# Kernel optimization log

Hardware: AMD Instinct MI355X
Metric: run time of the kernel (lower is better)

The kernel has to match this reference:

```python
import jax, jax.numpy as jnp
import numpy as np

N, E = 50000, 500000
SD, VD, HID, DEPTH = 128, 3, 64, 4
CUTOFF = 5.0


def setup_inputs() -> dict:
    key = jax.random.key(0)
    ks = jax.random.split(key, 13)
    s = jax.random.normal(ks[0], (N, SD), jnp.float32)
    v = jax.random.normal(ks[1], (N, VD, 3), jnp.float32)
    edge_index = jax.random.randint(ks[2], (2, E), 0, N, jnp.int32)
    d = jax.random.uniform(ks[3], (E, 1), jnp.float32) * CUTOFF  # distances within cutoff
    r = jax.random.normal(ks[4], (E, 3), jnp.float32)            # relative position vectors

    def lin(k, shp):
        return jax.random.normal(k, shp, jnp.float32) * (1.0 / np.sqrt(shp[-2]))

    # per-layer stacked parameters [DEPTH, ...]
    W1 = lin(ks[5], (DEPTH, 2 * SD + 1, HID)); b1 = jnp.zeros((DEPTH, HID), jnp.float32)
    W2 = lin(ks[6], (DEPTH, HID, HID));        b2 = jnp.zeros((DEPTH, HID), jnp.float32)
    W3 = lin(ks[7], (DEPTH, HID, SD + 2 * VD)); b3 = jnp.zeros((DEPTH, SD + 2 * VD), jnp.float32)
    Wn1 = lin(ks[8], (DEPTH, 2 * SD, HID)); bn1 = jnp.zeros((DEPTH, HID), jnp.float32)
    Wn2 = lin(ks[9], (DEPTH, HID, SD));     bn2 = jnp.zeros((DEPTH, SD), jnp.float32)
    return dict(s=s, v=v, edge_index=edge_index, d=d, r=r,
                W1=W1, b1=b1, W2=W2, b2=b2, W3=W3, b3=b3,
                Wn1=Wn1, bn1=bn1, Wn2=Wn2, bn2=bn2)


def _egnn(s, v, edge_index, d, r, W1, b1, W2, b2, W3, b3, Wn1, bn1, Wn2, bn2):
    dst, src = edge_index[0], edge_index[1]
    # cosine cutoff envelope, zero beyond CUTOFF
    C = 0.5 * (jnp.cos(jnp.pi * d / CUTOFF) + 1.0) * (d < CUTOFF)  # [E,1]
    # in-degree counts for 'mean' vector aggregation (fixed, layer-independent)
    cnt = jax.ops.segment_sum(jnp.ones((E,), jnp.float32), dst, num_segments=N)
    inv_cnt = 1.0 / jnp.maximum(cnt, 1.0)  # [N]
    for l in range(DEPTH):
        # gather + edge MLP (EGCL message)
        h = jnp.concatenate([s[dst], s[src], d], axis=-1)      # [E, 2*SD+1]
        h = jax.nn.silu(h @ W1[l] + b1[l])
        h = jax.nn.silu(h @ W2[l] + b2[l])
        m = h @ W3[l] + b3[l]                                   # [E, SD+2*VD]
        ms, gv, gr = m[:, :SD], m[:, SD:SD + VD], m[:, SD + VD:]
        ms = ms * C                                             # scalar message
        # equivariant vector message: gated source vectors + gated edge direction
        vm = (v[src] * gv[:, :, None] + r[:, None, :] * gr[:, :, None]) * C[:, :, None]
        # scatter aggregate: sum for scalars, mean for vectors (vector_aggr='mean')
        s_agg = jax.ops.segment_sum(ms, dst, num_segments=N)    # [N, SD]
        v_agg = jax.ops.segment_sum(vm, dst, num_segments=N) * inv_cnt[:, None, None]
        # node update (residual)
        u = jax.nn.silu(jnp.concatenate([s, s_agg], axis=-1) @ Wn1[l] + bn1[l])
        s = s + u @ Wn2[l] + bn2[l]
        v = v + v_agg
    return s, v


def reference(s, v, edge_index, d, r, W1, b1, W2, b2, W3, b3, Wn1, bn1, Wn2, bn2):
    return _egnn(s, v, edge_index, d, r, W1, b1, W2, b2, W3, b3, Wn1, bn1, Wn2, bn2)
```

## Files before the change

### kernel.cpp

```cpp
#include <hip/hip_runtime.h>
#include <hip/hip_bf16.h>
#include <math.h>

#define N_NODES 50000
#define N_EDGES 500000
#define SD 128
#define VD 3
#define HID 64
#define DEPTH 4

#define NF1 32
#define NF2 8
#define NF3 18
#define W1F_SH (NF1 * 512)
#define W2F_SH (NF2 * 512)
#define W3F_SH (NF3 * 512)
#define WPK_SH (W1F_SH + W2F_SH + W3F_SH)

#define WN1T_SH (64 * 256)
#define WN2T_SH (128 * 64)
#define WN_SH (WN1T_SH + WN2T_SH)

#define EDGE_GRID 512
#define NTILES (N_EDGES / 16)
#define EDGE_ITERS ((NTILES + EDGE_GRID * 4 - 1) / (EDGE_GRID * 4))

typedef __attribute__((ext_vector_type(8))) short short8;
typedef __attribute__((ext_vector_type(4))) float f32x4;

__device__ __forceinline__ float silu_f(float x) {
    return x / (1.0f + __expf(-x));
}

__device__ __forceinline__ unsigned short f2bf(float x) {
    __hip_bfloat16 h = __float2bfloat16(x);
    return *reinterpret_cast<unsigned short*>(&h);
}

__device__ __forceinline__ float bf2f(unsigned short u) {
    union { unsigned int i; float f; } c; c.i = ((unsigned int)u) << 16;
    return c.f;
}


__global__ void cast_s_kernel(const float* __restrict__ in, float* __restrict__ out,
                              unsigned short* __restrict__ out_bf, int n) {
    int i = blockIdx.x * blockDim.x + threadIdx.x;
    if (i < n) { float x = in[i]; out[i] = x; out_bf[i] = f2bf(x); }
}

__global__ void copy_kernel(const float* __restrict__ in, float* __restrict__ out, int n) {
    int i = blockIdx.x * blockDim.x + threadIdx.x;
    if (i < n) out[i] = in[i];
}

__global__ void prep_edges(const int* __restrict__ ei, const float* __restrict__ d,
                           float* __restrict__ C, int* __restrict__ cnti) {
    int e = blockIdx.x * blockDim.x + threadIdx.x;
    if (e >= N_EDGES) return;
    float de = d[e];
    float c = 0.5f * (cosf(3.14159265358979323846f * de * (1.0f / 5.0f)) + 1.0f);
    C[e] = (de < 5.0f) ? c : 0.0f;
    atomicAdd(&cnti[ei[e]], 1);
}

__global__ void inv_cnt_kernel(const int* __restrict__ cnti, float* __restrict__ inv_cnt) {
    int i = blockIdx.x * blockDim.x + threadIdx.x;
    if (i < N_NODES) inv_cnt[i] = 1.0f / fmaxf((float)cnti[i], 1.0f);
}

__global__ __launch_bounds__(1024) void scan_block(const int* __restrict__ cnti,
                                                   int* __restrict__ offs,
                                                   int* __restrict__ bsum) {
    __shared__ int sh[1024];
    int tid = threadIdx.x;
    int idx = blockIdx.x * 1024 + tid;
    int x = (idx < N_NODES) ? cnti[idx] : 0;
    sh[tid] = x;
    __syncthreads();
    for (int off = 1; off < 1024; off <<= 1) {
        int y = (tid >= off) ? sh[tid - off] : 0;
        __syncthreads();
        sh[tid] += y;
        __syncthreads();
    }
    if (idx < N_NODES) offs[idx] = sh[tid] - x;
    if (tid == 1023) bsum[blockIdx.x] = sh[1023];
}

__global__ void scan_partials(int* __restrict__ bsum, int nb, int* __restrict__ offs_total) {
    if (threadIdx.x == 0 && blockIdx.x == 0) {
        int acc = 0;
        for (int i = 0; i < nb; i++) { int t = bsum[i]; bsum[i] = acc; acc += t; }
        offs_total[0] = acc;
    }
}

__global__ __launch_bounds__(1024) void scan_apply(int* __restrict__ offs,
                                                   const int* __restrict__ bsum) {
    int idx = blockIdx.x * 1024 + threadIdx.x;
    if (idx < N_NODES) offs[idx] += bsum[blockIdx.x];
}

__global__ void build_perm(const int* __restrict__ ei, const int* __restrict__ offs,
                           int* __restrict__ cursor, int* __restrict__ eids) {
    int e = blockIdx.x * blockDim.x + threadIdx.x;
    if (e >= N_EDGES) return;
    int dst = ei[e];
    int p = offs[dst] + atomicAdd(&cursor[dst], 1);
    eids[p] = e;
}

__global__ void permute_edges(const int* __restrict__ ei, const float* __restrict__ d,
                              const float* __restrict__ C, const float* __restrict__ r,
                              const int* __restrict__ eids,
                              int* __restrict__ dst_s, int* __restrict__ src_s,
                              float* __restrict__ d_s, float* __restrict__ C_s,
                              float* __restrict__ r_s) {
    int p = blockIdx.x * blockDim.x + threadIdx.x;
    if (p >= N_EDGES) return;
    int e = eids[p];
    dst_s[p] = ei[e];
    src_s[p] = ei[N_EDGES + e];
    d_s[p] = d[e];
    C_s[p] = C[e];
    r_s[3 * (size_t)p + 0] = r[3 * (size_t)e + 0];
    r_s[3 * (size_t)p + 1] = r[3 * (size_t)e + 1];
    r_s[3 * (size_t)p + 2] = r[3 * (size_t)e + 2];
}

__global__ void prep_weights(const float* __restrict__ W1, const float* __restrict__ W2,
                             const float* __restrict__ W3, unsigned short* __restrict__ Wpk) {
    int idx = blockIdx.x * blockDim.x + threadIdx.x;
    if (idx >= DEPTH * WPK_SH) return;
    int l = idx / WPK_SH;
    int j = idx - l * WPK_SH;
    float val = 0.0f;
    if (j < W1F_SH) {
        int f = j >> 9, rrr = j & 511;
        int lane = rrr >> 3, jj = rrr & 7;
        int q = lane >> 4, lo = lane & 15;
        int ks = f >> 2, t = f & 3;
        int k = ks * 32 + q * 8 + jj;
        int n = t * 16 + lo;
        val = W1[((size_t)l * 257 + k) * 64 + n];
    } else if (j < W1F_SH + W2F_SH) {
        int jj2 = j - W1F_SH;
        int f = jj2 >> 9, rrr = jj2 & 511;
        int lane = rrr >> 3, jj = rrr & 7;
        int q = lane >> 4, lo = lane & 15;
        int ks = f >> 2, t = f & 3;
        int k = ks * 32 + q * 8 + jj;
        int n = t * 16 + lo;
        val = W2[((size_t)l * 64 + k) * 64 + n];
    } else {
        int jj3 = j - W1F_SH - W2F_SH;
        int f = jj3 >> 9, rrr = jj3 & 511;
        int lane = rrr >> 3, jj = rrr & 7;
        int q = lane >> 4, lo = lane & 15;
        int ks = f / 9, t = f - ks * 9;
        int k = ks * 32 + q * 8 + jj;
        int n = t * 16 + lo;
        val = (n < 134) ? W3[((size_t)l * 64 + k) * 134 + n] : 0.0f;
    }
    Wpk[idx] = f2bf(val);
}

__global__ void prep_node_weights(const float* __restrict__ Wn1, const float* __restrict__ Wn2,
                                  unsigned short* __restrict__ Wnpk) {
    int idx = blockIdx.x * blockDim.x + threadIdx.x;
    if (idx >= DEPTH * WN_SH) return;
    int l = idx / WN_SH;
    int j = idx - l * WN_SH;
    float val;
    if (j < WN1T_SH) {
        int n = j / 256, k = j - n * 256;
        val = Wn1[((size_t)l * 256 + k) * 64 + n];
    } else {
        int jj = j - WN1T_SH;
        int n = jj / 64, k = jj - n * 64;
        val = Wn2[((size_t)l * 64 + k) * 128 + n];
    }
    Wnpk[idx] = f2bf(val);
}

__global__ __launch_bounds__(256, 2) void edge_mfma(
    const unsigned short* __restrict__ s_bf, const float* __restrict__ v,
    const int* __restrict__ dst_s, const int* __restrict__ src_s,
    const float* __restrict__ d_s, const float* __restrict__ C_s,
    const float* __restrict__ r_s,
    const unsigned short* __restrict__ Wpk_l,
    const float* __restrict__ W1r,
    const float* __restrict__ b1, const float* __restrict__ b2,
    const float* __restrict__ b3,
    unsigned short* __restrict__ smsg, unsigned short* __restrict__ vmsg)
{
    __shared__ __align__(16) unsigned short w1f[W1F_SH];
    __shared__ __align__(16) unsigned short w3f[W3F_SH];
    __shared__ __align__(16) unsigned short Hb[4][16 * 72];
    __shared__ float gb[4][16][6];

    const int tid  = threadIdx.x;
    const int wl   = tid >> 6;
    const int lane = tid & 63;
    const int lo   = lane & 15;
    const int q    = lane >> 4;

    {
        const short8* g1 = reinterpret_cast<const short8*>(Wpk_l);
        const short8* g3 = reinterpret_cast<const short8*>(Wpk_l + W1F_SH + W2F_SH);
        short8* l1 = reinterpret_cast<short8*>(w1f);
        short8* l3 = reinterpret_cast<short8*>(w3f);
        for (int i = tid; i < W1F_SH / 8; i += 256) l1[i] = g1[i];
        for (int i = tid; i < W3F_SH / 8; i += 256) l3[i] = g3[i];
    }
    __syncthreads();

    const unsigned short* w2g = Wpk_l + W1F_SH;

    float bb1[4], wr1[4], bb2[4], bb3[9];
    #pragma unroll
    for (int t = 0; t < 4; t++) { bb1[t] = b1[t * 16 + lo]; wr1[t] = W1r[t * 16 + lo]; }
    #pragma unroll
    for (int t = 0; t < 4; t++) bb2[t] = b2[t * 16 + lo];
    #pragma unroll
    for (int t = 0; t < 9; t++) { int n = t * 16 + lo; bb3[t] = (n < 134) ? b3[n] : 0.0f; }

    int tile = blockIdx.x * 4 + wl;
    if (tile > NTILES - 1) tile = NTILES - 1;
    long eb = (long)tile * 16;
    int sn_t = 0;
    short8 ad[4], asf[4];
    float4 dd4, ce4;
    float vsr[9], rv[3], cel_t = 0.0f;
    {
        int dn = dst_s[eb + lo];
        int sn = src_s[eb + lo];
        dd4 = *reinterpret_cast<const float4*>(d_s + eb + 4 * q);
        ce4 = *reinterpret_cast<const float4*>(C_s + eb + 4 * q);
        const unsigned short* rd = s_bf + (size_t)dn * SD;
        const unsigned short* rs = s_bf + (size_t)sn * SD;
        #pragma unroll
        for (int ks = 0; ks < 4; ks++) {
            ad[ks]  = *reinterpret_cast<const short8*>(rd + ks * 32 + q * 8);
            asf[ks] = *reinterpret_cast<const short8*>(rs + ks * 32 + q * 8);
        }
        if (lane < 16) {
            sn_t = sn;
            cel_t = C_s[eb + lane];
            #pragma unroll
            for (int t = 0; t < 9; t++) vsr[t] = v[(size_t)sn * 9 + t];
            #pragma unroll
            for (int t = 0; t < 3; t++) rv[t] = r_s[3 * eb + 3 * lane + t];
        }
    }

    for (int it = 0; it < EDGE_ITERS; it++) {
        int tile_n = (it + 1) * (EDGE_GRID * 4) + blockIdx.x * 4 + wl;
        if (tile_n > NTILES - 1) tile_n = NTILES - 1;
        long ebn = (long)tile_n * 16;
        int dn_n = dst_s[ebn + lo];
        int sn_n = src_s[ebn + lo];
        float4 dd4_n = *reinterpret_cast<const float4*>(d_s + ebn + 4 * q);
        float4 ce4_n = *reinterpret_cast<const float4*>(C_s + ebn + 4 * q);
        float cel_n = 0.0f, rv_n[3];
        if (lane < 16) {
            cel_n = C_s[ebn + lane];
            #pragma unroll
            for (int t = 0; t < 3; t++) rv_n[t] = r_s[3 * ebn + 3 * lane + t];
        }

        f32x4 acc1[4];
        #pragma unroll
        for (int t = 0; t < 4; t++) {
            float dd[4] = { dd4.x, dd4.y, dd4.z, dd4.w };
            #pragma unroll
            for (int rr = 0; rr < 4; rr++) acc1[t][rr] = bb1[t] + dd[rr] * wr1[t];
        }
        #pragma unroll
        for (int ks = 0; ks < 4; ks++) {
            #pragma unroll
            for (int t = 0; t < 4; t++) {
                short8 b = *reinterpret_cast<const short8*>(&w1f[((ks * 4 + t) * 64 + lane) * 8]);
                acc1[t] = __builtin_amdgcn_mfma_f32_16x16x32_bf16(ad[ks], b, acc1[t], 0, 0, 0);
            }
        }
        #pragma unroll
        for (int ks = 0; ks < 4; ks++) {
            #pragma unroll
            for (int t = 0; t < 4; t++) {
                short8 b = *reinterpret_cast<const short8*>(&w1f[(((ks + 4) * 4 + t) * 64 + lane) * 8]);
                acc1[t] = __builtin_amdgcn_mfma_f32_16x16x32_bf16(asf[ks], b, acc1[t], 0, 0, 0);
            }
        }
        #pragma unroll
        for (int t = 0; t < 4; t++)
            #pragma unroll
            for (int rr = 0; rr < 4; rr++)
                Hb[wl][(4 * q + rr) * 72 + t * 16 + lo] = f2bf(silu_f(acc1[t][rr]));
        __syncthreads();

        short8 a2[2];
        #pragma unroll
        for (int ks = 0; ks < 2; ks++)
            a2[ks] = *reinterpret_cast<const short8*>(&Hb[wl][lo * 72 + ks * 32 + q * 8]);
        f32x4 acc2[4];
        #pragma unroll
        for (int t = 0; t < 4; t++) {
            #pragma unroll
            for (int rr = 0; rr < 4; rr++) acc2[t][rr] = bb2[t];
        }
        #pragma unroll
        for (int ks = 0; ks < 2; ks++) {
            #pragma unroll
            for (int t = 0; t < 4; t++) {
                short8 b = *reinterpret_cast<const short8*>(w2g + ((ks * 4 + t) * 64 + lane) * 8);
                acc2[t] = __builtin_amdgcn_mfma_f32_16x16x32_bf16(a2[ks], b, acc2[t], 0, 0, 0);
            }
        }

        short8 ad_n[4], as_n[4];
        {
            const unsigned short* rd = s_bf + (size_t)dn_n * SD;
            const unsigned short* rs = s_bf + (size_t)sn_n * SD;
            #pragma unroll
            for (int ks = 0; ks < 4; ks++) {
                ad_n[ks] = *reinterpret_cast<const short8*>(rd + ks * 32 + q * 8);
                as_n[ks] = *reinterpret_cast<const short8*>(rs + ks * 32 + q * 8);
            }
        }
        float vsr_n[9];
        if (lane < 16) {
            #pragma unroll
            for (int t = 0; t < 9; t++) vsr_n[t] = v[(size_t)sn_n * 9 + t];
        }

        __syncthreads();
        #pragma unroll
        for (int t = 0; t < 4; t++)
            #pragma unroll
            for (int rr = 0; rr < 4; rr++)
                Hb[wl][(4 * q + rr) * 72 + t * 16 + lo] = f2bf(silu_f(acc2[t][rr]));
        __syncthreads();

        short8 a3[2];
        #pragma unroll
        for (int ks = 0; ks < 2; ks++)
            a3[ks] = *reinterpret_cast<const short8*>(&Hb[wl][lo * 72 + ks * 32 + q * 8]);
        f32x4 acc3[9];
        #pragma unroll
        for (int t = 0; t < 9; t++) {
            #pragma unroll
            for (int rr = 0; rr < 4; rr++) acc3[t][rr] = bb3[t];
        }
        #pragma unroll
        for (int ks = 0; ks < 2; ks++) {
            #pragma unroll
            for (int t = 0; t < 9; t++) {
                short8 b = *reinterpret_cast<const short8*>(&w3f[((ks * 9 + t) * 64 + lane) * 8]);
                acc3[t] = __builtin_amdgcn_mfma_f32_16x16x32_bf16(a3[ks], b, acc3[t], 0, 0, 0);
            }
        }

        float ce[4] = { ce4.x, ce4.y, ce4.z, ce4.w };
        #pragma unroll
        for (int t = 0; t < 8; t++) {
            int colc = t * 16 + lo;
            #pragma unroll
            for (int rr = 0; rr < 4; rr++) {
                long erow = eb + 4 * q + rr;
                smsg[erow * SD + colc] = f2bf(acc3[t][rr] * ce[rr]);
            }
        }
        if (lo < 6) {
            #pragma unroll
            for (int rr = 0; rr < 4; rr++) gb[wl][4 * q + rr][lo] = acc3[8][rr];
        }
        __syncthreads();

        if (lane < 16) {
            long e = eb + lane;
            #pragma unroll
            for (int vi = 0; vi < VD; vi++) {
                float gv = gb[wl][lane][vi], gr = gb[wl][lane][VD + vi];
                vmsg[e * 12 + vi * 3 + 0] = f2bf((vsr[vi * 3 + 0] * gv + rv[0] * gr) * cel_t);
                vmsg[e * 12 + vi * 3 + 1] = f2bf((vsr[vi * 3 + 1] * gv + rv[1] * gr) * cel_t);
                vmsg[e * 12 + vi * 3 + 2] = f2bf((vsr[vi * 3 + 2] * gv + rv[2] * gr) * cel_t);
            }
        }

        eb = ebn;
        dd4 = dd4_n; ce4 = ce4_n;
        cel_t = cel_n; sn_t = sn_n;
        #pragma unroll
        for (int ks = 0; ks < 4; ks++) { ad[ks] = ad_n[ks]; asf[ks] = as_n[ks]; }
        #pragma unroll
        for (int t = 0; t < 9; t++) vsr[t] = vsr_n[t];
        #pragma unroll
        for (int t = 0; t < 3; t++) rv[t] = rv_n[t];
    }
}

__global__ __launch_bounds__(256) void agg_kernel(
    const unsigned short* __restrict__ smsg, const unsigned short* __restrict__ vmsg,
    const int* __restrict__ offs,
    unsigned short* __restrict__ s_agg_bf, float* __restrict__ v_agg)
{
    int wave = blockIdx.x * 4 + (threadIdx.x >> 6);
    int lane = threadIdx.x & 63;
    if (wave >= N_NODES) return;
    int beg = offs[wave], end = offs[wave + 1];
    float a0 = 0.0f, a1 = 0.0f, va = 0.0f;
    const ushort2* sm2 = reinterpret_cast<const ushort2*>(smsg);
    for (int i = beg; i < end; i++) {
        ushort2 mm = sm2[(size_t)i * 64 + lane];
        a0 += bf2f(mm.x);
        a1 += bf2f(mm.y);
        if (lane < 9) va += bf2f(vmsg[(size_t)i * 12 + lane]);
    }
    ushort2 o; o.x = f2bf(a0); o.y = f2bf(a1);
    *reinterpret_cast<ushort2*>(s_agg_bf + (size_t)wave * SD + lane * 2) = o;
    if (lane < 9) v_agg[(size_t)wave * 9 + lane] = va;
}

__global__ __launch_bounds__(256) void node_mfma(
    float* __restrict__ s, float* __restrict__ v, unsigned short* __restrict__ s_bf,
    const unsigned short* __restrict__ s_agg_bf, const float* __restrict__ v_agg,
    const float* __restrict__ inv_cnt,
    const unsigned short* __restrict__ Wn_l,
    const float* __restrict__ bn1, const float* __restrict__ bn2)
{
    __shared__ __align__(16) unsigned short Hb[4][16 * 72];

    const int tid  = threadIdx.x;
    const int wl   = tid >> 6;
    const int lane = tid & 63;
    const int lo   = lane & 15;
    const int q    = lane >> 4;
    const int nb   = blockIdx.x * 64 + wl * 16;

    int na = nb + lo; if (na > N_NODES - 1) na = N_NODES - 1;
    const unsigned short* rs = s_bf     + (size_t)na * SD;
    const unsigned short* ra = s_agg_bf + (size_t)na * SD;

    f32x4 acc1[4];
    #pragma unroll
    for (int t = 0; t < 4; t++) {
        float bb = bn1[t * 16 + lo];
        #pragma unroll
        for (int rr = 0; rr < 4; rr++) acc1[t][rr] = bb;
    }
    #pragma unroll
    for (int ks = 0; ks < 4; ks++) {
        short8 a = *reinterpret_cast<const short8*>(rs + ks * 32 + q * 8);
        #pragma unroll
        for (int t = 0; t < 4; t++) {
            short8 b = *reinterpret_cast<const short8*>(Wn_l + (t * 16 + lo) * 256 + ks * 32 + q * 8);
            acc1[t] = __builtin_amdgcn_mfma_f32_16x16x32_bf16(a, b, acc1[t], 0, 0, 0);
        }
    }
    #pragma unroll
    for (int ks = 0; ks < 4; ks++) {
        short8 a = *reinterpret_cast<const short8*>(ra + ks * 32 + q * 8);
        #pragma unroll
        for (int t = 0; t < 4; t++) {
            short8 b = *reinterpret_cast<const short8*>(Wn_l + (t * 16 + lo) * 256 + 128 + ks * 32 + q * 8);
            acc1[t] = __builtin_amdgcn_mfma_f32_16x16x32_bf16(a, b, acc1[t], 0, 0, 0);
        }
    }
    #pragma unroll
    for (int t = 0; t < 4; t++)
        #pragma unroll
        for (int rr = 0; rr < 4; rr++)
            Hb[wl][(4 * q + rr) * 72 + t * 16 + lo] = f2bf(silu_f(acc1[t][rr]));
    __syncthreads();

    const unsigned short* w2g = Wn_l + WN1T_SH;
    f32x4 acc2[8];
    #pragma unroll
    for (int t = 0; t < 8; t++) {
        float bb = bn2[t * 16 + lo];
        #pragma unroll
        for (int rr = 0; rr < 4; rr++) acc2[t][rr] = bb;
    }
    #pragma unroll
    for (int ks = 0; ks < 2; ks++) {
        short8 a = *reinterpret_cast<const short8*>(&Hb[wl][lo * 72 + ks * 32 + q * 8]);
        #pragma unroll
        for (int t = 0; t < 8; t++) {
            short8 b = *reinterpret_cast<const short8*>(w2g + (t * 16 + lo) * 64 + ks * 32 + q * 8);
            acc2[t] = __builtin_amdgcn_mfma_f32_16x16x32_bf16(a, b, acc2[t], 0, 0, 0);
        }
    }

    #pragma unroll
    for (int t = 0; t < 8; t++) {
        int col = t * 16 + lo;
        #pragma unroll
        for (int rr = 0; rr < 4; rr++) {
            int node = nb + 4 * q + rr;
            if (node < N_NODES) {
                size_t idx = (size_t)node * SD + col;
                float ns = s[idx] + acc2[t][rr];
                s[idx] = ns;
                s_bf[idx] = f2bf(ns);
            }
        }
    }

    if (lane < 16) {
        int node = nb + lane;
        if (node < N_NODES) {
            float ic = inv_cnt[node];
            #pragma unroll
            for (int t = 0; t < VD * 3; t++)
                v[(size_t)node * 9 + t] += v_agg[(size_t)node * 9 + t] * ic;
        }
    }
}

extern "C" void kernel_launch(void* const* d_in, const int* in_sizes, int n_in,
                              void* d_out, int out_size, void* d_ws, size_t ws_size,
                              hipStream_t stream)
{
    (void)in_sizes; (void)n_in; (void)out_size; (void)ws_size;
    const float* s_in = (const float*)d_in[0];
    const float* v_in = (const float*)d_in[1];
    const int*   ei   = (const int*)d_in[2];
    const float* d_e  = (const float*)d_in[3];
    const float* r_e  = (const float*)d_in[4];
    const float* W1   = (const float*)d_in[5];
    const float* b1   = (const float*)d_in[6];
    const float* W2   = (const float*)d_in[7];
    const float* b2   = (const float*)d_in[8];
    const float* W3   = (const float*)d_in[9];
    const float* b3   = (const float*)d_in[10];
    const float* Wn1  = (const float*)d_in[11];
    const float* bn1  = (const float*)d_in[12];
    const float* Wn2  = (const float*)d_in[13];
    const float* bn2  = (const float*)d_in[14];

    float* s = (float*)d_out;
    float* v = s + (size_t)N_NODES * SD;

    float* ws      = (float*)d_ws;
    float* v_agg   = ws;
    float* cntinv  = v_agg + (size_t)N_NODES * 9;
    float* Cbuf    = cntinv + N_NODES;
    int*   cnti    = (int*)(Cbuf + N_EDGES);
    int*   offs    = cnti + N_NODES;
    int*   cursor  = offs + N_NODES + 1;
    int*   eids    = cursor + N_NODES;
    int*   bsum    = eids + N_EDGES;
    int*   dst_s   = bsum + 64;
    int*   src_s   = dst_s + N_EDGES;
    float* d_s     = (float*)(src_s + N_EDGES);
    float* C_s     = d_s + N_EDGES;
    float* r_s     = C_s + N_EDGES;
    uintptr_t up   = (uintptr_t)(r_s + (size_t)3 * N_EDGES);
    up = (up + 15) & ~(uintptr_t)15;
    unsigned short* s_bf     = (unsigned short*)up;
    unsigned short* s_agg_bf = s_bf + (size_t)N_NODES * SD;
    unsigned short* Wpk      = s_agg_bf + (size_t)N_NODES * SD;
    unsigned short* Wnpk     = Wpk + (size_t)DEPTH * WPK_SH;
    unsigned short* smsg     = Wnpk + (size_t)DEPTH * WN_SH;
    unsigned short* vmsg     = smsg + (size_t)N_EDGES * SD;

    hipMemsetAsync(cnti, 0, sizeof(int) * (size_t)N_NODES, stream);
    hipMemsetAsync(cursor, 0, sizeof(int) * (size_t)N_NODES, stream);

    cast_s_kernel<<<(N_NODES * SD + 255) / 256, 256, 0, stream>>>(s_in, s, s_bf, N_NODES * SD);
    copy_kernel<<<(N_NODES * VD * 3 + 255) / 256, 256, 0, stream>>>(v_in, v, N_NODES * VD * 3);
    prep_edges<<<(N_EDGES + 255) / 256, 256, 0, stream>>>(ei, d_e, Cbuf, cnti);
    inv_cnt_kernel<<<(N_NODES + 255) / 256, 256, 0, stream>>>(cnti, cntinv);

    const int NB = (N_NODES + 1023) / 1024;
    scan_block<<<NB, 1024, 0, stream>>>(cnti, offs, bsum);
    scan_partials<<<1, 64, 0, stream>>>(bsum, NB, offs + N_NODES);
    scan_apply<<<NB, 1024, 0, stream>>>(offs, bsum);
    build_perm<<<(N_EDGES + 255) / 256, 256, 0, stream>>>(ei, offs, cursor, eids);
    permute_edges<<<(N_EDGES + 255) / 256, 256, 0, stream>>>(
        ei, d_e, Cbuf, r_e, eids, dst_s, src_s, d_s, C_s, r_s);

    prep_weights<<<(DEPTH * WPK_SH + 255) / 256, 256, 0, stream>>>(W1, W2, W3, Wpk);
    prep_node_weights<<<(DEPTH * WN_SH + 255) / 256, 256, 0, stream>>>(Wn1, Wn2, Wnpk);

    for (int l = 0; l < DEPTH; l++) {
        edge_mfma<<<EDGE_GRID, 256, 0, stream>>>(
            s_bf, v, dst_s, src_s, d_s, C_s, r_s,
            Wpk + (size_t)l * WPK_SH,
            W1 + ((size_t)l * 257 + 256) * 64,
            b1 + (size_t)l * HID, b2 + (size_t)l * HID, b3 + (size_t)l * (SD + 2 * VD),
            smsg, vmsg);
        agg_kernel<<<(N_NODES + 3) / 4, 256, 0, stream>>>(
            smsg, vmsg, offs, s_agg_bf, v_agg);
        node_mfma<<<(N_NODES + 63) / 64, 256, 0, stream>>>(
            s, v, s_bf, s_agg_bf, v_agg, cntinv,
            Wnpk + (size_t)l * WN_SH,
            bn1 + (size_t)l * HID, bn2 + (size_t)l * SD);
    }
}
```

Baseline: 954.9 us.

## Fuse message aggregation into edge kernel with segmented atomic adds

The edge kernel now reduces each 16-edge tile's scalar and vector messages by runs of equal destination node (edges are sorted by dst) and adds them straight into fp32 s_agg/v_agg with atomics. This removes the separate aggregation kernel and the bf16 per-edge message buffers written to and read back from global memory. The aggregate buffer is zeroed each layer with a memset, and the node kernel converts the fp32 aggregate to bf16 on load. In exchange it adds extra block barriers, atomic traffic and a serial segment loop per tile, and the order of the floating-point summation is no longer fixed.

```diff
diff --git a/kernel.cpp b/kernel.cpp
--- a/kernel.cpp
+++ b/kernel.cpp
@@ -40,6 +40,13 @@
 __device__ __forceinline__ float bf2f(unsigned short u) {
     union { unsigned int i; float f; } c; c.i = ((unsigned int)u) << 16;
     return c.f;
+}
+
+__device__ __forceinline__ short8 cvt8(const float* __restrict__ p) {
+    short8 o;
+    #pragma unroll
+    for (int i = 0; i < 8; i++) o[i] = (short)f2bf(p[i]);
+    return o;
 }
 
 
@@ -193,12 +200,14 @@
     const float* __restrict__ W1r,
     const float* __restrict__ b1, const float* __restrict__ b2,
     const float* __restrict__ b3,
-    unsigned short* __restrict__ smsg, unsigned short* __restrict__ vmsg)
+    float* __restrict__ s_agg, float* __restrict__ v_agg)
 {
     __shared__ __align__(16) unsigned short w1f[W1F_SH];
     __shared__ __align__(16) unsigned short w3f[W3F_SH];
     __shared__ __align__(16) unsigned short Hb[4][16 * 72];
     __shared__ float gb[4][16][6];
+    __shared__ float vtile[4][16][9];
+    __shared__ int tdst[4][16];
 
     const int tid  = threadIdx.x;
     const int wl   = tid >> 6;
@@ -226,19 +235,19 @@
     #pragma unroll
     for (int t = 0; t < 9; t++) { int n = t * 16 + lo; bb3[t] = (n < 134) ? b3[n] : 0.0f; }
 
-    int tile = blockIdx.x * 4 + wl;
-    if (tile > NTILES - 1) tile = NTILES - 1;
-    long eb = (long)tile * 16;
-    int sn_t = 0;
+    int raw0 = blockIdx.x * 4 + wl;
+    bool val_c = true;
+    long eb = (long)raw0 * 16;
+    int dn_c;
     short8 ad[4], asf[4];
     float4 dd4, ce4;
     float vsr[9], rv[3], cel_t = 0.0f;
     {
-        int dn = dst_s[eb + lo];
+        dn_c = dst_s[eb + lo];
         int sn = src_s[eb + lo];
         dd4 = *reinterpret_cast<const float4*>(d_s + eb + 4 * q);
         ce4 = *reinterpret_cast<const float4*>(C_s + eb + 4 * q);
-        const unsigned short* rd = s_bf + (size_t)dn * SD;
+        const unsigned short* rd = s_bf + (size_t)dn_c * SD;
         const unsigned short* rs = s_bf + (size_t)sn * SD;
         #pragma unroll
         for (int ks = 0; ks < 4; ks++) {
@@ -246,7 +255,6 @@
             asf[ks] = *reinterpret_cast<const short8*>(rs + ks * 32 + q * 8);
         }
         if (lane < 16) {
-            sn_t = sn;
             cel_t = C_s[eb + lane];
             #pragma unroll
             for (int t = 0; t < 9; t++) vsr[t] = v[(size_t)sn * 9 + t];
@@ -256,8 +264,9 @@
     }
 
     for (int it = 0; it < EDGE_ITERS; it++) {
-        int tile_n = (it + 1) * (EDGE_GRID * 4) + blockIdx.x * 4 + wl;
-        if (tile_n > NTILES - 1) tile_n = NTILES - 1;
+        int raw_n = (it + 1) * (EDGE_GRID * 4) + blockIdx.x * 4 + wl;
+        bool val_n = (raw_n < NTILES);
+        int tile_n = val_n ? raw_n : (NTILES - 1);
         long ebn = (long)tile_n * 16;
         int dn_n = dst_s[ebn + lo];
         int sn_n = src_s[ebn + lo];
@@ -362,36 +371,58 @@
             }
         }
 
-        float ce[4] = { ce4.x, ce4.y, ce4.z, ce4.w };
-        #pragma unroll
-        for (int t = 0; t < 8; t++) {
-            int colc = t * 16 + lo;
-            #pragma unroll
-            for (int rr = 0; rr < 4; rr++) {
-                long erow = eb + 4 * q + rr;
-                smsg[erow * SD + colc] = f2bf(acc3[t][rr] * ce[rr]);
-            }
-        }
         if (lo < 6) {
             #pragma unroll
             for (int rr = 0; rr < 4; rr++) gb[wl][4 * q + rr][lo] = acc3[8][rr];
         }
+        if (lane < 16) tdst[wl][lane] = dn_c;
         __syncthreads();
 
         if (lane < 16) {
-            long e = eb + lane;
             #pragma unroll
             for (int vi = 0; vi < VD; vi++) {
                 float gv = gb[wl][lane][vi], gr = gb[wl][lane][VD + vi];
-                vmsg[e * 12 + vi * 3 + 0] = f2bf((vsr[vi * 3 + 0] * gv + rv[0] * gr) * cel_t);
-                vmsg[e * 12 + vi * 3 + 1] = f2bf((vsr[vi * 3 + 1] * gv + rv[1] * gr) * cel_t);
-                vmsg[e * 12 + vi * 3 + 2] = f2bf((vsr[vi * 3 + 2] * gv + rv[2] * gr) * cel_t);
-            }
-        }
-
+                vtile[wl][lane][vi * 3 + 0] = (vsr[vi * 3 + 0] * gv + rv[0] * gr) * cel_t;
+                vtile[wl][lane][vi * 3 + 1] = (vsr[vi * 3 + 1] * gv + rv[1] * gr) * cel_t;
+                vtile[wl][lane][vi * 3 + 2] = (vsr[vi * 3 + 2] * gv + rv[2] * gr) * cel_t;
+            }
+        }
+        __syncthreads();
+
+        if (val_c) {
+            float ce[4] = { ce4.x, ce4.y, ce4.z, ce4.w };
+            int sseg = 0;
+            while (sseg < 16) {
+                int dnode = tdst[wl][sseg];
+                int eseg = sseg + 1;
+                while (eseg < 16 && tdst[wl][eseg] == dnode) eseg++;
+                float* srow = s_agg + (size_t)dnode * SD;
+                #pragma unroll
+                for (int t = 0; t < 8; t++) {
+                    float p = 0.0f;
+                    #pragma unroll
+                    for (int rr = 0; rr < 4; rr++) {
+                        int row = 4 * q + rr;
+                        p += (row >= sseg && row < eseg) ? acc3[t][rr] * ce[rr] : 0.0f;
+                    }
+                    p += __shfl_xor(p, 16);
+                    p += __shfl_xor(p, 32);
+                    if (q == 0) atomicAdd(&srow[t * 16 + lo], p);
+                }
+                if (lane < 9) {
+                    float pv = 0.0f;
+                    for (int i = sseg; i < eseg; i++) pv += vtile[wl][i][lane];
+                    atomicAdd(&v_agg[(size_t)dnode * 9 + lane], pv);
+                }
+                sseg = eseg;
+            }
+        }
+
+        val_c = val_n;
         eb = ebn;
+        dn_c = dn_n;
         dd4 = dd4_n; ce4 = ce4_n;
-        cel_t = cel_n; sn_t = sn_n;
+        cel_t = cel_n;
         #pragma unroll
         for (int ks = 0; ks < 4; ks++) { ad[ks] = ad_n[ks]; asf[ks] = as_n[ks]; }
         #pragma unroll
@@ -399,33 +430,11 @@
         #pragma unroll
         for (int t = 0; t < 3; t++) rv[t] = rv_n[t];
     }
-}
-
-__global__ __launch_bounds__(256) void agg_kernel(
-    const unsigned short* __restrict__ smsg, const unsigned short* __restrict__ vmsg,
-    const int* __restrict__ offs,
-    unsigned short* __restrict__ s_agg_bf, float* __restrict__ v_agg)
-{
-    int wave = blockIdx.x * 4 + (threadIdx.x >> 6);
-    int lane = threadIdx.x & 63;
-    if (wave >= N_NODES) return;
-    int beg = offs[wave], end = offs[wave + 1];
-    float a0 = 0.0f, a1 = 0.0f, va = 0.0f;
-    const ushort2* sm2 = reinterpret_cast<const ushort2*>(smsg);
-    for (int i = beg; i < end; i++) {
-        ushort2 mm = sm2[(size_t)i * 64 + lane];
-        a0 += bf2f(mm.x);
-        a1 += bf2f(mm.y);
-        if (lane < 9) va += bf2f(vmsg[(size_t)i * 12 + lane]);
-    }
-    ushort2 o; o.x = f2bf(a0); o.y = f2bf(a1);
-    *reinterpret_cast<ushort2*>(s_agg_bf + (size_t)wave * SD + lane * 2) = o;
-    if (lane < 9) v_agg[(size_t)wave * 9 + lane] = va;
 }
 
 __global__ __launch_bounds__(256) void node_mfma(
     float* __restrict__ s, float* __restrict__ v, unsigned short* __restrict__ s_bf,
-    const unsigned short* __restrict__ s_agg_bf, const float* __restrict__ v_agg,
+    const float* __restrict__ s_agg, const float* __restrict__ v_agg,
     const float* __restrict__ inv_cnt,
     const unsigned short* __restrict__ Wn_l,
     const float* __restrict__ bn1, const float* __restrict__ bn2)
@@ -440,8 +449,8 @@
     const int nb   = blockIdx.x * 64 + wl * 16;
 
     int na = nb + lo; if (na > N_NODES - 1) na = N_NODES - 1;
-    const unsigned short* rs = s_bf     + (size_t)na * SD;
-    const unsigned short* ra = s_agg_bf + (size_t)na * SD;
+    const unsigned short* rs = s_bf  + (size_t)na * SD;
+    const float*          ra = s_agg + (size_t)na * SD;
 
     f32x4 acc1[4];
     #pragma unroll
@@ -461,7 +470,7 @@
     }
     #pragma unroll
     for (int ks = 0; ks < 4; ks++) {
-        short8 a = *reinterpret_cast<const short8*>(ra + ks * 32 + q * 8);
+        short8 a = cvt8(ra + ks * 32 + q * 8);
         #pragma unroll
         for (int t = 0; t < 4; t++) {
             short8 b = *reinterpret_cast<const short8*>(Wn_l + (t * 16 + lo) * 256 + 128 + ks * 32 + q * 8);
@@ -544,7 +553,8 @@
     float* v = s + (size_t)N_NODES * SD;
 
     float* ws      = (float*)d_ws;
-    float* v_agg   = ws;
+    float* s_agg   = ws;
+    float* v_agg   = s_agg + (size_t)N_NODES * SD;
     float* cntinv  = v_agg + (size_t)N_NODES * 9;
     float* Cbuf    = cntinv + N_NODES;
     int*   cnti    = (int*)(Cbuf + N_EDGES);
@@ -559,12 +569,9 @@
     float* r_s     = C_s + N_EDGES;
     uintptr_t up   = (uintptr_t)(r_s + (size_t)3 * N_EDGES);
     up = (up + 15) & ~(uintptr_t)15;
-    unsigned short* s_bf     = (unsigned short*)up;
-    unsigned short* s_agg_bf = s_bf + (size_t)N_NODES * SD;
-    unsigned short* Wpk      = s_agg_bf + (size_t)N_NODES * SD;
-    unsigned short* Wnpk     = Wpk + (size_t)DEPTH * WPK_SH;
-    unsigned short* smsg     = Wnpk + (size_t)DEPTH * WN_SH;
-    unsigned short* vmsg     = smsg + (size_t)N_EDGES * SD;
+    unsigned short* s_bf = (unsigned short*)up;
+    unsigned short* Wpk  = s_bf + (size_t)N_NODES * SD;
+    unsigned short* Wnpk = Wpk + (size_t)DEPTH * WPK_SH;
 
     hipMemsetAsync(cnti, 0, sizeof(int) * (size_t)N_NODES, stream);
     hipMemsetAsync(cursor, 0, sizeof(int) * (size_t)N_NODES, stream);
@@ -586,16 +593,15 @@
     prep_node_weights<<<(DEPTH * WN_SH + 255) / 256, 256, 0, stream>>>(Wn1, Wn2, Wnpk);
 
     for (int l = 0; l < DEPTH; l++) {
+        hipMemsetAsync(s_agg, 0, sizeof(float) * (size_t)N_NODES * (SD + 9), stream);
         edge_mfma<<<EDGE_GRID, 256, 0, stream>>>(
             s_bf, v, dst_s, src_s, d_s, C_s, r_s,
             Wpk + (size_t)l * WPK_SH,
             W1 + ((size_t)l * 257 + 256) * 64,
             b1 + (size_t)l * HID, b2 + (size_t)l * HID, b3 + (size_t)l * (SD + 2 * VD),
-            smsg, vmsg);
-        agg_kernel<<<(N_NODES + 3) / 4, 256, 0, stream>>>(
-            smsg, vmsg, offs, s_agg_bf, v_agg);
+            s_agg, v_agg);
         node_mfma<<<(N_NODES + 63) / 64, 256, 0, stream>>>(
-            s, v, s_bf, s_agg_bf, v_agg, cntinv,
+            s, v, s_bf, s_agg, v_agg, cntinv,
             Wnpk + (size_t)l * WN_SH,
             bn1 + (size_t)l * HID, bn2 + (size_t)l * SD);
     }
```

Measured after the change: 1.076 ms. 1.13x slower.
